# Kernel optimization log

Measured on AMD Instinct MI355X. Metric: run time of the kernel, lower is better.

## Reference

```python
import jax, jax.numpy as jnp
import numpy as np

C = 256
HEADS = 8
HEAD_DIM = C // HEADS
GROUPS = 8
EPS = 1e-5


def setup_inputs() -> dict:
    key = jax.random.key(0)
    ks = jax.random.split(key, 11)
    B, S = 2, 16
    s = 0.02
    return {
        "x": jax.random.normal(ks[0], (B, C, S, S, S), dtype=jnp.float32),
        "gn_w": jnp.ones((C,), jnp.float32),
        "gn_b": jnp.zeros((C,), jnp.float32),
        "wq": jax.random.normal(ks[1], (C, C), jnp.float32) * s,
        "bq": jnp.zeros((C,), jnp.float32),
        "wk": jax.random.normal(ks[2], (C, C), jnp.float32) * s,
        "bk": jnp.zeros((C,), jnp.float32),
        "wv": jax.random.normal(ks[3], (C, C), jnp.float32) * s,
        "bv": jnp.zeros((C,), jnp.float32),
        "wo": jax.random.normal(ks[4], (C, C), jnp.float32) * s,
        "bo": jnp.zeros((C,), jnp.float32),
    }


def _group_norm(x, w, b):
    # x: [B, C, D, H, W]; GroupNorm(8, C) with affine params
    B, Cc, D, H, W = x.shape
    xg = x.reshape(B, GROUPS, Cc // GROUPS, D, H, W)
    mu = jnp.mean(xg, axis=(2, 3, 4, 5), keepdims=True)
    var = jnp.mean(jnp.square(xg - mu), axis=(2, 3, 4, 5), keepdims=True)
    xn = ((xg - mu) * jax.lax.rsqrt(var + EPS)).reshape(B, Cc, D, H, W)
    return xn * w[None, :, None, None, None] + b[None, :, None, None, None]


def reference(x, gn_w, gn_b, wq, bq, wk, bk, wv, bv, wo, bo):
    B, Cc, D, H, W = x.shape
    N = D * H * W
    xn = _group_norm(x, gn_w, gn_b).reshape(B, Cc, N)  # [B,C,N]
    # 1x1x1 Conv3d == per-voxel linear: weight [out,in]
    Q = jnp.einsum("oc,bcn->bon", wq, xn) + bq[None, :, None]
    K = jnp.einsum("oc,bcn->bon", wk, xn) + bk[None, :, None]
    V = jnp.einsum("oc,bcn->bon", wv, xn) + bv[None, :, None]
    Q = Q.reshape(B, HEADS, HEAD_DIM, N)
    K = K.reshape(B, HEADS, HEAD_DIM, N)
    V = V.reshape(B, HEADS, HEAD_DIM, N)
    scale = np.sqrt(HEAD_DIM).astype(np.float32)
    attn = jnp.einsum("bhdn,bhdm->bhnm", Q, K) / scale
    attn = jax.nn.softmax(attn, axis=-1)
    out = jnp.einsum("bhnm,bhdm->bhdn", attn, V)  # [B,h,hd,N]
    out = out.reshape(B, Cc, N)
    out = jnp.einsum("oc,bcn->bon", wo, out) + bo[None, :, None]
    return x + out.reshape(B, Cc, D, H, W)
```

## Files before the change

kernel.cpp:

```cpp
#include <hip/hip_runtime.h>

#define B_   2
#define C_   256
#define N_   4096
#define H_   8
#define HD_  32
#define G_   8
#define CPG_ 32

typedef short short8 __attribute__((ext_vector_type(8)));
typedef short short4v __attribute__((ext_vector_type(4)));
typedef unsigned uint4v __attribute__((ext_vector_type(4)));
typedef float f32x4  __attribute__((ext_vector_type(4)));
typedef float f4     __attribute__((ext_vector_type(4)));

__device__ __forceinline__ float b2f(short s) {
    return __uint_as_float(((unsigned)(unsigned short)s) << 16);
}
__device__ __forceinline__ short f2b(float f) {
    unsigned u = __float_as_uint(f);
    unsigned r = (u + 0x7FFF + ((u >> 16) & 1)) >> 16;
    return (short)r;
}

__global__ __launch_bounds__(256) void gn_part(const float* __restrict__ x,
                                               float* __restrict__ part) {
    int blk = blockIdx.x;
    const f4* p = (const f4*)x + (size_t)(blk >> 6) * (CPG_ * N_ / 4) + (size_t)(blk & 63) * 512;
    float s = 0.f, ss = 0.f;
#pragma unroll
    for (int i = 0; i < 2; i++) {
        f4 v = p[threadIdx.x + i * 256];
#pragma unroll
        for (int j = 0; j < 4; j++) { float f = v[j]; s += f; ss += f * f; }
    }
#pragma unroll
    for (int off = 32; off > 0; off >>= 1) {
        s  += __shfl_down(s, off);
        ss += __shfl_down(ss, off);
    }
    __shared__ float rs[4], rss[4];
    int w = threadIdx.x >> 6;
    if ((threadIdx.x & 63) == 0) { rs[w] = s; rss[w] = ss; }
    __syncthreads();
    if (threadIdx.x == 0) {
        part[blk * 2]     = rs[0] + rs[1] + rs[2] + rs[3];
        part[blk * 2 + 1] = rss[0] + rss[1] + rss[2] + rss[3];
    }
}

__global__ __launch_bounds__(256) void gemm_qkv(
    const float* __restrict__ x,
    const float* __restrict__ gw, const float* __restrict__ gb,
    const float* __restrict__ part,
    const float* __restrict__ wq, const float* __restrict__ bq,
    const float* __restrict__ wk, const float* __restrict__ bk,
    const float* __restrict__ wv, const float* __restrict__ bv,
    short* __restrict__ q, short* __restrict__ kt, short* __restrict__ v) {
    int z = blockIdx.z;
    int b = z / 3, which = z % 3;
    const float* W    = which == 0 ? wq : (which == 1 ? wk : wv);
    const float* bias = which == 0 ? bq : (which == 1 ? bk : bv);
    bool trans = (which != 2);
    float mul = (which == 0) ? (0.17677669529663687f * 1.4426950408889634f) : 1.0f;

    __shared__ short wl[64][40];
    __shared__ short xl[128][40];
    __shared__ float ga[256], gbb[256];
    __shared__ float mus[8], rstds[8];

    int o0 = blockIdx.y * 64, n0 = blockIdx.x * 128;
    int tid = threadIdx.x;
    int w = tid >> 6, lane = tid & 63, li = lane & 15, quad = lane >> 4;
    int wr = w & 1, wc = w >> 1;

#pragma unroll
    for (int gi = 0; gi < 2; gi++) {
        int g = w * 2 + gi;
        const float* pp = &part[(size_t)(b * 8 + g) * 128 + lane * 2];
        float s = pp[0], ss = pp[1];
#pragma unroll
        for (int off = 32; off > 0; off >>= 1) {
            s  += __shfl_down(s, off);
            ss += __shfl_down(ss, off);
        }
        if (lane == 0) {
            const float inv = 1.f / (float)(CPG_ * N_);
            float mu = s * inv;
            float var = ss * inv - mu * mu;
            mus[g] = mu;
            rstds[g] = rsqrtf(var + 1e-5f);
        }
    }
    __syncthreads();
    {
        int c = tid, g = c >> 5;
        float a = rstds[g] * gw[c];
        ga[c]  = a;
        gbb[c] = gb[c] - mus[g] * a;
    }

    f32x4 acc[8];
#pragma unroll
    for (int i = 0; i < 8; i++) acc[i] = (f32x4){0.f, 0.f, 0.f, 0.f};

    int cpair = tid >> 4, l16 = tid & 15;
    __syncthreads();

    for (int k0 = 0; k0 < 256; k0 += 32) {
        {
            int row = tid >> 2, co = (tid & 3) << 3;
            const float* wp = &W[(size_t)(o0 + row) * 256 + k0 + co];
            f4 wa = *(const f4*)wp;
            f4 wb = *(const f4*)(wp + 4);
            short8 w8;
#pragma unroll
            for (int j = 0; j < 4; j++) { w8[j] = f2b(wa[j]); w8[j + 4] = f2b(wb[j]); }
            *(short8*)&wl[row][co] = w8;
        }
        {
            int c0 = k0 + cpair * 2;
            float a0 = ga[c0],     b0c = gbb[c0];
            float a1 = ga[c0 + 1], b1c = gbb[c0 + 1];
            const float* xr0 = x + ((size_t)(b * 256 + c0)) * N_ + n0 + l16;
            const float* xr1 = xr0 + N_;
#pragma unroll
            for (int j = 0; j < 8; j++) {
                unsigned lo = (unsigned short)f2b(xr0[16 * j] * a0 + b0c);
                unsigned hi = (unsigned short)f2b(xr1[16 * j] * a1 + b1c);
                *(unsigned*)&xl[l16 + 16 * j][cpair * 2] = lo | (hi << 16);
            }
        }
        __syncthreads();
        short8 af[4], bfr[4];
        if (trans) {
#pragma unroll
            for (int i = 0; i < 4; i++) af[i]  = *(short8*)&xl[wr * 64 + i * 16 + li][quad * 8];
#pragma unroll
            for (int j = 0; j < 2; j++) bfr[j] = *(short8*)&wl[wc * 32 + j * 16 + li][quad * 8];
#pragma unroll
            for (int i = 0; i < 4; i++)
#pragma unroll
                for (int j = 0; j < 2; j++)
                    acc[i * 2 + j] = __builtin_amdgcn_mfma_f32_16x16x32_bf16(af[i], bfr[j], acc[i * 2 + j], 0, 0, 0);
        } else {
#pragma unroll
            for (int i = 0; i < 2; i++) af[i]  = *(short8*)&wl[wr * 32 + i * 16 + li][quad * 8];
#pragma unroll
            for (int j = 0; j < 4; j++) bfr[j] = *(short8*)&xl[wc * 64 + j * 16 + li][quad * 8];
#pragma unroll
            for (int i = 0; i < 2; i++)
#pragma unroll
                for (int j = 0; j < 4; j++)
                    acc[i * 4 + j] = __builtin_amdgcn_mfma_f32_16x16x32_bf16(af[i], bfr[j], acc[i * 4 + j], 0, 0, 0);
        }
        __syncthreads();
    }

    if (which == 2) {
        short* outp = v + (size_t)b * C_ * N_;
#pragma unroll
        for (int i = 0; i < 2; i++) {
            int ob = o0 + wr * 32 + i * 16 + quad * 4;
#pragma unroll
            for (int j = 0; j < 4; j++) {
                int n_ = n0 + wc * 64 + j * 16 + li;
#pragma unroll
                for (int r = 0; r < 4; r++) {
                    float val = acc[i * 4 + j][r] + bias[ob + r];
                    outp[(size_t)(ob + r) * N_ + n_] = f2b(val);
                }
            }
        }
    } else if (which == 0) {
        short* outp = q + (size_t)b * N_ * C_;
#pragma unroll
        for (int i = 0; i < 4; i++) {
            int nb_ = n0 + wr * 64 + i * 16 + quad * 4;
#pragma unroll
            for (int j = 0; j < 2; j++) {
                int o_ = o0 + wc * 32 + j * 16 + li;
                float bv_ = bias[o_];
#pragma unroll
                for (int r = 0; r < 4; r++)
                    outp[(size_t)(nb_ + r) * C_ + o_] = f2b((acc[i * 2 + j][r] + bv_) * mul);
            }
        }
    } else {
#pragma unroll
        for (int i = 0; i < 4; i++) {
            int nb_ = n0 + wr * 64 + i * 16 + quad * 4;
#pragma unroll
            for (int j = 0; j < 2; j++) {
                int o_ = o0 + wc * 32 + j * 16 + li;
                int hh = o_ >> 5, d = o_ & 31;
                float bv_ = bias[o_];
                short* kdst = kt + ((size_t)(b * 8 + hh) * N_) * HD_ + d;
#pragma unroll
                for (int r = 0; r < 4; r++)
                    kdst[(size_t)(nb_ + r) * HD_] = f2b(acc[i * 2 + j][r] + bv_);
            }
        }
    }
}

__global__ __launch_bounds__(512) void flash(const short* __restrict__ q,
                                             const short* __restrict__ ktp,
                                             const short* __restrict__ v,
                                             float* __restrict__ Opart,
                                             float* __restrict__ lrbuf,
                                             int nsplit, int nt) {
    int bid = blockIdx.x;
    int xcd = bid & 7;
    int rest = bid >> 3;
    int bh = xcd * 2 + (rest & 1);
    int r2 = rest >> 1;
    int nb = r2 & 15;
    int qt = r2 >> 4;
    int b = bh >> 3, h = bh & 7;
    int moff = qt * (N_ / nsplit);

    const short* QT = q   + (size_t)b * N_ * C_ + h * HD_;
    const short* KP = ktp + (size_t)bh * N_ * HD_ + (size_t)moff * HD_;
    const short* V  = v   + ((size_t)b * C_ + h * HD_) * N_ + moff;
    const size_t TS = (size_t)B_ * N_ * C_;
    float* Oh  = Opart + (size_t)qt * TS + (size_t)b * N_ * C_ + h * HD_;
    float* lrp = lrbuf + ((size_t)qt * 16 + bh) * N_;

    __shared__ short kl[2 * 2560];
    __shared__ short vl[2 * 2560];

    int tid = threadIdx.x, w = tid >> 6, lane = tid & 63, li = lane & 15, quad = lane >> 4;
    int n0w = nb * 256 + w * 32;

    short8 qf0 = *(const short8*)&QT[(size_t)(n0w + li) * 256 + quad * 8];
    short8 qf1 = *(const short8*)&QT[(size_t)(n0w + 16 + li) * 256 + quad * 8];

    f32x4 oa00 = (f32x4){0.f,0.f,0.f,0.f}, oa01 = oa00, oa10 = oa00, oa11 = oa00;
    float lr0 = 0.f, lr1 = 0.f;
    const f32x4 zero = (f32x4){0.f, 0.f, 0.f, 0.f};

    int krow = tid >> 3, kcol = (tid & 7) << 2;
    const short* kgp = KP + (size_t)krow * HD_ + kcol;
    int klo = krow * 40 + kcol;
    int vd = tid >> 4, g = tid & 15;
    int mbase = 32 * (g >> 3) + 16 * (g & 1) + 4 * ((g >> 1) & 3);
    const short* vgp = V + (size_t)vd * N_ + mbase;
    int vlo = (vd + 32 * (g >> 3)) * 40 + 4 * (g & 7);

    short4v kst = *(const short4v*)kgp;
    short4v vst = *(const short4v*)vgp;

    f32x4 s0[4], s1[4];
    short8 vf[4];

    for (int t = 0; t < nt; ++t) {
        int buf = t & 1;
        *(short4v*)&kl[buf * 2560 + klo] = kst;
        *(short4v*)&vl[buf * 2560 + vlo] = vst;
        if (t < nt - 1) {
            kst = *(const short4v*)(kgp + (size_t)(t + 1) * 64 * HD_);
            vst = *(const short4v*)(vgp + (t + 1) * 64);
        }
        __syncthreads();

        __builtin_amdgcn_s_setprio(1);
#pragma unroll
        for (int c = 0; c < 4; c++) {
            short8 kf = *(short8*)&kl[buf * 2560 + (c * 16 + li) * 40 + quad * 8];
            s0[c] = __builtin_amdgcn_mfma_f32_16x16x32_bf16(kf, qf0, zero, 0, 0, 0);
            s1[c] = __builtin_amdgcn_mfma_f32_16x16x32_bf16(kf, qf1, zero, 0, 0, 0);
        }
        __builtin_amdgcn_s_setprio(0);

        vf[0] = *(short8*)&vl[buf * 2560 + li * 40 + quad * 8];
        vf[1] = *(short8*)&vl[buf * 2560 + (16 + li) * 40 + quad * 8];
        vf[2] = *(short8*)&vl[buf * 2560 + (32 + li) * 40 + quad * 8];
        vf[3] = *(short8*)&vl[buf * 2560 + (48 + li) * 40 + quad * 8];

        unsigned paw[8];
        float lp = 0.f;
#pragma unroll
        for (int c = 0; c < 4; c++) {
            float e0 = __builtin_amdgcn_exp2f(s0[c][0]);
            float e1 = __builtin_amdgcn_exp2f(s0[c][1]);
            float e2 = __builtin_amdgcn_exp2f(s0[c][2]);
            float e3 = __builtin_amdgcn_exp2f(s0[c][3]);
            lp += (e0 + e1) + (e2 + e3);
            paw[2 * c]     = __builtin_amdgcn_perm(__float_as_uint(e1), __float_as_uint(e0), 0x07060302);
            paw[2 * c + 1] = __builtin_amdgcn_perm(__float_as_uint(e3), __float_as_uint(e2), 0x07060302);
        }
        lr0 += lp;
        uint4v p0 = (uint4v){paw[0], paw[1], paw[2], paw[3]};
        uint4v p1 = (uint4v){paw[4], paw[5], paw[6], paw[7]};
        short8 a0 = __builtin_bit_cast(short8, p0);
        short8 a1 = __builtin_bit_cast(short8, p1);

        lp = 0.f;
#pragma unroll
        for (int c = 0; c < 4; c++) {
            float e0 = __builtin_amdgcn_exp2f(s1[c][0]);
            float e1 = __builtin_amdgcn_exp2f(s1[c][1]);
            float e2 = __builtin_amdgcn_exp2f(s1[c][2]);
            float e3 = __builtin_amdgcn_exp2f(s1[c][3]);
            lp += (e0 + e1) + (e2 + e3);
            paw[2 * c]     = __builtin_amdgcn_perm(__float_as_uint(e1), __float_as_uint(e0), 0x07060302);
            paw[2 * c + 1] = __builtin_amdgcn_perm(__float_as_uint(e3), __float_as_uint(e2), 0x07060302);
        }
        lr1 += lp;
        uint4v p2 = (uint4v){paw[0], paw[1], paw[2], paw[3]};
        uint4v p3 = (uint4v){paw[4], paw[5], paw[6], paw[7]};
        short8 a2 = __builtin_bit_cast(short8, p2);
        short8 a3 = __builtin_bit_cast(short8, p3);

        __builtin_amdgcn_s_setprio(1);
        oa00 = __builtin_amdgcn_mfma_f32_16x16x32_bf16(a0, vf[0], oa00, 0, 0, 0);
        oa01 = __builtin_amdgcn_mfma_f32_16x16x32_bf16(a0, vf[1], oa01, 0, 0, 0);
        oa00 = __builtin_amdgcn_mfma_f32_16x16x32_bf16(a1, vf[2], oa00, 0, 0, 0);
        oa01 = __builtin_amdgcn_mfma_f32_16x16x32_bf16(a1, vf[3], oa01, 0, 0, 0);
        oa10 = __builtin_amdgcn_mfma_f32_16x16x32_bf16(a2, vf[0], oa10, 0, 0, 0);
        oa11 = __builtin_amdgcn_mfma_f32_16x16x32_bf16(a2, vf[1], oa11, 0, 0, 0);
        oa10 = __builtin_amdgcn_mfma_f32_16x16x32_bf16(a3, vf[2], oa10, 0, 0, 0);
        oa11 = __builtin_amdgcn_mfma_f32_16x16x32_bf16(a3, vf[3], oa11, 0, 0, 0);
        __builtin_amdgcn_s_setprio(0);
    }

    lr0 += __shfl_xor(lr0, 16); lr0 += __shfl_xor(lr0, 32);
    lr1 += __shfl_xor(lr1, 16); lr1 += __shfl_xor(lr1, 32);
#pragma unroll
    for (int r = 0; r < 4; r++) {
        size_t n_ = (size_t)(n0w + quad * 4 + r);
        Oh[n_ * 256 + li]      = oa00[r];
        Oh[n_ * 256 + 16 + li] = oa01[r];
        size_t n2 = (size_t)(n0w + 16 + quad * 4 + r);
        Oh[n2 * 256 + li]      = oa10[r];
        Oh[n2 * 256 + 16 + li] = oa11[r];
    }
    if (quad == 0) {
        lrp[n0w + li]      = lr0;
        lrp[n0w + 16 + li] = lr1;
    }
}

__global__ __launch_bounds__(256) void combine(const float* __restrict__ Opart,
                                               const float* __restrict__ lrbuf,
                                               short* __restrict__ aoT,
                                               int nsplit) {
    int idx = blockIdx.x * 256 + threadIdx.x;
    int cg = idx & 31;
    int n  = (idx >> 5) & 4095;
    int b  = idx >> 17;
    int c0 = cg * 8;
    int bh = b * 8 + (c0 >> 5);
    const size_t TS = (size_t)B_ * N_ * C_;
    float l = 0.f;
    for (int qt = 0; qt < nsplit; ++qt)
        l += lrbuf[((size_t)qt * 16 + bh) * N_ + n];
    float inv = 1.f / l;
    size_t base = ((size_t)b * N_ + n) * 256 + c0;
    f4 a0 = (f4){0.f,0.f,0.f,0.f}, a1 = a0;
    for (int qt = 0; qt < nsplit; ++qt) {
        const float* p = Opart + (size_t)qt * TS + base;
        a0 += *(const f4*)p;
        a1 += *(const f4*)(p + 4);
    }
    short8 r;
#pragma unroll
    for (int j = 0; j < 4; j++) {
        r[j]     = f2b(a0[j] * inv);
        r[j + 4] = f2b(a1[j] * inv);
    }
    *(short8*)&aoT[base] = r;
}

__global__ __launch_bounds__(256) void gemm_out(const float* __restrict__ W,
                                                const float* __restrict__ bias,
                                                const short* __restrict__ aoT,
                                                const float* __restrict__ resid,
                                                float* __restrict__ out) {
    int b = blockIdx.z;
    const short* X = aoT + (size_t)b * N_ * C_;
    const float* R = resid + (size_t)b * C_ * N_;
    float* outp = out + (size_t)b * C_ * N_;

    __shared__ short wl[128][40];
    __shared__ short xl[64][40];

    int o0 = blockIdx.y * 128, n0 = blockIdx.x * 64;
    int tid = threadIdx.x;
    int w = tid >> 6, lane = tid & 63, li = lane & 15, quad = lane >> 4;
    int wr = w & 1, wc = w >> 1;

    f32x4 acc[4][2];
#pragma unroll
    for (int i = 0; i < 4; i++)
#pragma unroll
        for (int j = 0; j < 2; j++) acc[i][j] = (f32x4){0.f, 0.f, 0.f, 0.f};

    for (int k0 = 0; k0 < 256; k0 += 32) {
#pragma unroll
        for (int i = 0; i < 2; i++) {
            int idx = tid + i * 256;
            int row = idx >> 2, co = (idx & 3) << 3;
            const float* wp = &W[(size_t)(o0 + row) * 256 + k0 + co];
            f4 wa = *(const f4*)wp;
            f4 wb = *(const f4*)(wp + 4);
            short8 w8;
#pragma unroll
            for (int j = 0; j < 4; j++) { w8[j] = f2b(wa[j]); w8[j + 4] = f2b(wb[j]); }
            *(short8*)&wl[row][co] = w8;
        }
        {
            int row = tid >> 2, co = (tid & 3) << 3;
            *(short8*)&xl[row][co] = *(const short8*)&X[(size_t)(n0 + row) * 256 + k0 + co];
        }
        __syncthreads();
        short8 af[4], bfr[2];
#pragma unroll
        for (int i = 0; i < 4; i++) af[i]  = *(short8*)&wl[wr * 64 + i * 16 + li][quad * 8];
#pragma unroll
        for (int j = 0; j < 2; j++) bfr[j] = *(short8*)&xl[wc * 32 + j * 16 + li][quad * 8];
#pragma unroll
        for (int i = 0; i < 4; i++)
#pragma unroll
            for (int j = 0; j < 2; j++)
                acc[i][j] = __builtin_amdgcn_mfma_f32_16x16x32_bf16(af[i], bfr[j], acc[i][j], 0, 0, 0);
        __syncthreads();
    }
#pragma unroll
    for (int i = 0; i < 4; i++) {
        int ob = o0 + wr * 64 + i * 16 + quad * 4;
#pragma unroll
        for (int j = 0; j < 2; j++) {
            int n_ = n0 + wc * 32 + j * 16 + li;
#pragma unroll
            for (int r = 0; r < 4; r++) {
                size_t idx = (size_t)(ob + r) * N_ + n_;
                outp[idx] = acc[i][j][r] + bias[ob + r] + R[idx];
            }
        }
    }
}

extern "C" void kernel_launch(void* const* d_in, const int* in_sizes, int n_in,
                              void* d_out, int out_size, void* d_ws, size_t ws_size,
                              hipStream_t stream) {
    const float* x  = (const float*)d_in[0];
    const float* gw = (const float*)d_in[1];
    const float* gb = (const float*)d_in[2];
    const float* wq = (const float*)d_in[3];
    const float* bq = (const float*)d_in[4];
    const float* wk = (const float*)d_in[5];
    const float* bk = (const float*)d_in[6];
    const float* wv = (const float*)d_in[7];
    const float* bv = (const float*)d_in[8];
    const float* wo = (const float*)d_in[9];
    const float* bo = (const float*)d_in[10];
    float* out = (float*)d_out;

    char* ws = (char*)d_ws;
    float* part = (float*)ws;
    const size_t TS = (size_t)B_ * N_ * C_;
    short* aoT = (short*)(ws + 16384);
    short* q   = aoT + TS;
    short* kt  = q + TS;
    short* v   = kt + TS;
    float* Of  = (float*)(v + TS);
    const int SP = 2;
    float* lr  = Of + (size_t)SP * TS;

    gn_part<<<1024, 256, 0, stream>>>(x, part);
    gemm_qkv<<<dim3(32, 4, 6), 256, 0, stream>>>(x, gw, gb, part,
                                                 wq, bq, wk, bk, wv, bv, q, kt, v);
    flash<<<SP * 256, 512, 0, stream>>>(q, kt, v, Of, lr, SP, (N_ / SP) / 64);
    combine<<<1024, 256, 0, stream>>>(Of, lr, aoT, SP);
    gemm_out<<<dim3(64, 2, 2), 256, 0, stream>>>(wo, bo, aoT, x, out);
}
```

Baseline: 149.1 us.

## Software-pipeline flash PV across iterations, relayout V tile, shrink out-GEMM tile

The flash loop now overlaps work across iterations: the PV MFMAs for tile t-1 are issued alongside the QK MFMAs for tile t, while the exp/pack of P moves after them. A prologue and epilogue handle the first and last tiles. The V shared-memory tile gets a new 72-stride layout, and launch bounds request 2 blocks per CU. Separately, gemm_out uses a 64-row output tile with twice as many blocks to raise occupancy, at the cost of more redundant loads of X.

```diff
diff --git a/kernel.cpp b/kernel.cpp
--- a/kernel.cpp
+++ b/kernel.cpp
@@ -204,12 +204,43 @@
     }
 }
 
-__global__ __launch_bounds__(512) void flash(const short* __restrict__ q,
-                                             const short* __restrict__ ktp,
-                                             const short* __restrict__ v,
-                                             float* __restrict__ Opart,
-                                             float* __restrict__ lrbuf,
-                                             int nsplit, int nt) {
+#define EXPPACK(sx, lrx, A0, A1)                                          \
+    {                                                                     \
+        unsigned paw[8];                                                  \
+        float lp = 0.f;                                                   \
+        _Pragma("unroll")                                                 \
+        for (int c = 0; c < 4; c++) {                                     \
+            float e0 = __builtin_amdgcn_exp2f(sx[c][0]);                  \
+            float e1 = __builtin_amdgcn_exp2f(sx[c][1]);                  \
+            float e2 = __builtin_amdgcn_exp2f(sx[c][2]);                  \
+            float e3 = __builtin_amdgcn_exp2f(sx[c][3]);                  \
+            lp += (e0 + e1) + (e2 + e3);                                  \
+            paw[2 * c]     = __builtin_amdgcn_perm(__float_as_uint(e1), __float_as_uint(e0), 0x07060302); \
+            paw[2 * c + 1] = __builtin_amdgcn_perm(__float_as_uint(e3), __float_as_uint(e2), 0x07060302); \
+        }                                                                 \
+        lrx += lp;                                                        \
+        uint4v p0_ = (uint4v){paw[0], paw[1], paw[2], paw[3]};            \
+        uint4v p1_ = (uint4v){paw[4], paw[5], paw[6], paw[7]};            \
+        A0 = __builtin_bit_cast(short8, p0_);                             \
+        A1 = __builtin_bit_cast(short8, p1_);                             \
+    }
+
+#define PV8(P0, P1, P2, P3, V0, V1, V2, V3)                               \
+    oa00 = __builtin_amdgcn_mfma_f32_16x16x32_bf16(P0, V0, oa00, 0, 0, 0); \
+    oa01 = __builtin_amdgcn_mfma_f32_16x16x32_bf16(P0, V1, oa01, 0, 0, 0); \
+    oa00 = __builtin_amdgcn_mfma_f32_16x16x32_bf16(P1, V2, oa00, 0, 0, 0); \
+    oa01 = __builtin_amdgcn_mfma_f32_16x16x32_bf16(P1, V3, oa01, 0, 0, 0); \
+    oa10 = __builtin_amdgcn_mfma_f32_16x16x32_bf16(P2, V0, oa10, 0, 0, 0); \
+    oa11 = __builtin_amdgcn_mfma_f32_16x16x32_bf16(P2, V1, oa11, 0, 0, 0); \
+    oa10 = __builtin_amdgcn_mfma_f32_16x16x32_bf16(P3, V2, oa10, 0, 0, 0); \
+    oa11 = __builtin_amdgcn_mfma_f32_16x16x32_bf16(P3, V3, oa11, 0, 0, 0);
+
+__global__ __launch_bounds__(512, 2) void flash(const short* __restrict__ q,
+                                                const short* __restrict__ ktp,
+                                                const short* __restrict__ v,
+                                                float* __restrict__ Opart,
+                                                float* __restrict__ lrbuf,
+                                                int nsplit, int nt) {
     int bid = blockIdx.x;
     int xcd = bid & 7;
     int rest = bid >> 3;
@@ -228,7 +259,7 @@
     float* lrp = lrbuf + ((size_t)qt * 16 + bh) * N_;
 
     __shared__ short kl[2 * 2560];
-    __shared__ short vl[2 * 2560];
+    __shared__ short vl[2 * 2304];
 
     int tid = threadIdx.x, w = tid >> 6, lane = tid & 63, li = lane & 15, quad = lane >> 4;
     int n0w = nb * 256 + w * 32;
@@ -246,18 +277,37 @@
     int vd = tid >> 4, g = tid & 15;
     int mbase = 32 * (g >> 3) + 16 * (g & 1) + 4 * ((g >> 1) & 3);
     const short* vgp = V + (size_t)vd * N_ + mbase;
-    int vlo = (vd + 32 * (g >> 3)) * 40 + 4 * (g & 7);
+    int vlo = vd * 72 + g * 4;
 
     short4v kst = *(const short4v*)kgp;
     short4v vst = *(const short4v*)vgp;
 
     f32x4 s0[4], s1[4];
-    short8 vf[4];
-
-    for (int t = 0; t < nt; ++t) {
+    short8 vfp0, vfp1, vfp2, vfp3;
+    short8 pap0, pap1, pap2, pap3;
+
+    *(short4v*)&kl[klo] = kst;
+    *(short4v*)&vl[vlo] = vst;
+    kst = *(const short4v*)(kgp + (size_t)64 * HD_);
+    vst = *(const short4v*)(vgp + 64);
+    __syncthreads();
+#pragma unroll
+    for (int c = 0; c < 4; c++) {
+        short8 kf = *(short8*)&kl[(c * 16 + li) * 40 + quad * 8];
+        s0[c] = __builtin_amdgcn_mfma_f32_16x16x32_bf16(kf, qf0, zero, 0, 0, 0);
+        s1[c] = __builtin_amdgcn_mfma_f32_16x16x32_bf16(kf, qf1, zero, 0, 0, 0);
+    }
+    vfp0 = *(short8*)&vl[li * 72 + quad * 8];
+    vfp1 = *(short8*)&vl[(16 + li) * 72 + quad * 8];
+    vfp2 = *(short8*)&vl[li * 72 + 32 + quad * 8];
+    vfp3 = *(short8*)&vl[(16 + li) * 72 + 32 + quad * 8];
+    EXPPACK(s0, lr0, pap0, pap1);
+    EXPPACK(s1, lr1, pap2, pap3);
+
+    for (int t = 1; t < nt; ++t) {
         int buf = t & 1;
         *(short4v*)&kl[buf * 2560 + klo] = kst;
-        *(short4v*)&vl[buf * 2560 + vlo] = vst;
+        *(short4v*)&vl[buf * 2304 + vlo] = vst;
         if (t < nt - 1) {
             kst = *(const short4v*)(kgp + (size_t)(t + 1) * 64 * HD_);
             vst = *(const short4v*)(vgp + (t + 1) * 64);
@@ -271,59 +321,24 @@
             s0[c] = __builtin_amdgcn_mfma_f32_16x16x32_bf16(kf, qf0, zero, 0, 0, 0);
             s1[c] = __builtin_amdgcn_mfma_f32_16x16x32_bf16(kf, qf1, zero, 0, 0, 0);
         }
+
+        short8 vfc0 = *(short8*)&vl[buf * 2304 + li * 72 + quad * 8];
+        short8 vfc1 = *(short8*)&vl[buf * 2304 + (16 + li) * 72 + quad * 8];
+        short8 vfc2 = *(short8*)&vl[buf * 2304 + li * 72 + 32 + quad * 8];
+        short8 vfc3 = *(short8*)&vl[buf * 2304 + (16 + li) * 72 + 32 + quad * 8];
+
+        PV8(pap0, pap1, pap2, pap3, vfp0, vfp1, vfp2, vfp3);
         __builtin_amdgcn_s_setprio(0);
 
-        vf[0] = *(short8*)&vl[buf * 2560 + li * 40 + quad * 8];
-        vf[1] = *(short8*)&vl[buf * 2560 + (16 + li) * 40 + quad * 8];
-        vf[2] = *(short8*)&vl[buf * 2560 + (32 + li) * 40 + quad * 8];
-        vf[3] = *(short8*)&vl[buf * 2560 + (48 + li) * 40 + quad * 8];
-
-        unsigned paw[8];
-        float lp = 0.f;
-#pragma unroll
-        for (int c = 0; c < 4; c++) {
-            float e0 = __builtin_amdgcn_exp2f(s0[c][0]);
-            float e1 = __builtin_amdgcn_exp2f(s0[c][1]);
-            float e2 = __builtin_amdgcn_exp2f(s0[c][2]);
-            float e3 = __builtin_amdgcn_exp2f(s0[c][3]);
-            lp += (e0 + e1) + (e2 + e3);
-            paw[2 * c]     = __builtin_amdgcn_perm(__float_as_uint(e1), __float_as_uint(e0), 0x07060302);
-            paw[2 * c + 1] = __builtin_amdgcn_perm(__float_as_uint(e3), __float_as_uint(e2), 0x07060302);
-        }
-        lr0 += lp;
-        uint4v p0 = (uint4v){paw[0], paw[1], paw[2], paw[3]};
-        uint4v p1 = (uint4v){paw[4], paw[5], paw[6], paw[7]};
-        short8 a0 = __builtin_bit_cast(short8, p0);
-        short8 a1 = __builtin_bit_cast(short8, p1);
-
-        lp = 0.f;
-#pragma unroll
-        for (int c = 0; c < 4; c++) {
-            float e0 = __builtin_amdgcn_exp2f(s1[c][0]);
-            float e1 = __builtin_amdgcn_exp2f(s1[c][1]);
-            float e2 = __builtin_amdgcn_exp2f(s1[c][2]);
-            float e3 = __builtin_amdgcn_exp2f(s1[c][3]);
-            lp += (e0 + e1) + (e2 + e3);
-            paw[2 * c]     = __builtin_amdgcn_perm(__float_as_uint(e1), __float_as_uint(e0), 0x07060302);
-            paw[2 * c + 1] = __builtin_amdgcn_perm(__float_as_uint(e3), __float_as_uint(e2), 0x07060302);
-        }
-        lr1 += lp;
-        uint4v p2 = (uint4v){paw[0], paw[1], paw[2], paw[3]};
-        uint4v p3 = (uint4v){paw[4], paw[5], paw[6], paw[7]};
-        short8 a2 = __builtin_bit_cast(short8, p2);
-        short8 a3 = __builtin_bit_cast(short8, p3);
-
-        __builtin_amdgcn_s_setprio(1);
-        oa00 = __builtin_amdgcn_mfma_f32_16x16x32_bf16(a0, vf[0], oa00, 0, 0, 0);
-        oa01 = __builtin_amdgcn_mfma_f32_16x16x32_bf16(a0, vf[1], oa01, 0, 0, 0);
-        oa00 = __builtin_amdgcn_mfma_f32_16x16x32_bf16(a1, vf[2], oa00, 0, 0, 0);
-        oa01 = __builtin_amdgcn_mfma_f32_16x16x32_bf16(a1, vf[3], oa01, 0, 0, 0);
-        oa10 = __builtin_amdgcn_mfma_f32_16x16x32_bf16(a2, vf[0], oa10, 0, 0, 0);
-        oa11 = __builtin_amdgcn_mfma_f32_16x16x32_bf16(a2, vf[1], oa11, 0, 0, 0);
-        oa10 = __builtin_amdgcn_mfma_f32_16x16x32_bf16(a3, vf[2], oa10, 0, 0, 0);
-        oa11 = __builtin_amdgcn_mfma_f32_16x16x32_bf16(a3, vf[3], oa11, 0, 0, 0);
-        __builtin_amdgcn_s_setprio(0);
-    }
+        EXPPACK(s0, lr0, pap0, pap1);
+        EXPPACK(s1, lr1, pap2, pap3);
+
+        vfp0 = vfc0; vfp1 = vfc1; vfp2 = vfc2; vfp3 = vfc3;
+    }
+
+    __builtin_amdgcn_s_setprio(1);
+    PV8(pap0, pap1, pap2, pap3, vfp0, vfp1, vfp2, vfp3);
+    __builtin_amdgcn_s_setprio(0);
 
     lr0 += __shfl_xor(lr0, 16); lr0 += __shfl_xor(lr0, 32);
     lr1 += __shfl_xor(lr1, 16); lr1 += __shfl_xor(lr1, 32);
@@ -383,25 +398,23 @@
     const float* R = resid + (size_t)b * C_ * N_;
     float* outp = out + (size_t)b * C_ * N_;
 
-    __shared__ short wl[128][40];
+    __shared__ short wl[64][40];
     __shared__ short xl[64][40];
 
-    int o0 = blockIdx.y * 128, n0 = blockIdx.x * 64;
+    int o0 = blockIdx.y * 64, n0 = blockIdx.x * 64;
     int tid = threadIdx.x;
     int w = tid >> 6, lane = tid & 63, li = lane & 15, quad = lane >> 4;
     int wr = w & 1, wc = w >> 1;
 
-    f32x4 acc[4][2];
-#pragma unroll
-    for (int i = 0; i < 4; i++)
+    f32x4 acc[2][2];
+#pragma unroll
+    for (int i = 0; i < 2; i++)
 #pragma unroll
         for (int j = 0; j < 2; j++) acc[i][j] = (f32x4){0.f, 0.f, 0.f, 0.f};
 
+    int row = tid >> 2, co = (tid & 3) << 3;
     for (int k0 = 0; k0 < 256; k0 += 32) {
-#pragma unroll
-        for (int i = 0; i < 2; i++) {
-            int idx = tid + i * 256;
-            int row = idx >> 2, co = (idx & 3) << 3;
+        {
             const float* wp = &W[(size_t)(o0 + row) * 256 + k0 + co];
             f4 wa = *(const f4*)wp;
             f4 wb = *(const f4*)(wp + 4);
@@ -410,26 +423,23 @@
             for (int j = 0; j < 4; j++) { w8[j] = f2b(wa[j]); w8[j + 4] = f2b(wb[j]); }
             *(short8*)&wl[row][co] = w8;
         }
-        {
-            int row = tid >> 2, co = (tid & 3) << 3;
-            *(short8*)&xl[row][co] = *(const short8*)&X[(size_t)(n0 + row) * 256 + k0 + co];
-        }
+        *(short8*)&xl[row][co] = *(const short8*)&X[(size_t)(n0 + row) * 256 + k0 + co];
         __syncthreads();
-        short8 af[4], bfr[2];
-#pragma unroll
-        for (int i = 0; i < 4; i++) af[i]  = *(short8*)&wl[wr * 64 + i * 16 + li][quad * 8];
+        short8 af[2], bfr[2];
+#pragma unroll
+        for (int i = 0; i < 2; i++) af[i]  = *(short8*)&wl[wr * 32 + i * 16 + li][quad * 8];
 #pragma unroll
         for (int j = 0; j < 2; j++) bfr[j] = *(short8*)&xl[wc * 32 + j * 16 + li][quad * 8];
 #pragma unroll
-        for (int i = 0; i < 4; i++)
+        for (int i = 0; i < 2; i++)
 #pragma unroll
             for (int j = 0; j < 2; j++)
                 acc[i][j] = __builtin_amdgcn_mfma_f32_16x16x32_bf16(af[i], bfr[j], acc[i][j], 0, 0, 0);
         __syncthreads();
     }
 #pragma unroll
-    for (int i = 0; i < 4; i++) {
-        int ob = o0 + wr * 64 + i * 16 + quad * 4;
+    for (int i = 0; i < 2; i++) {
+        int ob = o0 + wr * 32 + i * 16 + quad * 4;
 #pragma unroll
         for (int j = 0; j < 2; j++) {
             int n_ = n0 + wc * 32 + j * 16 + li;
@@ -474,5 +484,5 @@
                                                  wq, bq, wk, bk, wv, bv, q, kt, v);
     flash<<<SP * 256, 512, 0, stream>>>(q, kt, v, Of, lr, SP, (N_ / SP) / 64);
     combine<<<1024, 256, 0, stream>>>(Of, lr, aoT, SP);
-    gemm_out<<<dim3(64, 2, 2), 256, 0, stream>>>(wo, bo, aoT, x, out);
-}
+    gemm_out<<<dim3(64, 4, 2), 256, 0, stream>>>(wo, bo, aoT, x, out);
+}
```

Result: no change. 150.4 us (+0.9%).
